# Performance work log

Hardware: AMD Instinct MI355X
Metric: run time of the kernel (lower is better)

The kernel has to match this reference:

```python
import jax, jax.numpy as jnp
import numpy as np

D_MODEL = 256
D_CLIP = 768
NHEAD = 8
HEAD_DIM = D_MODEL // NHEAD
Q_LEN = 100
B = 32
T_LEN = 1203


def setup_inputs() -> dict:
    key = jax.random.key(0)
    ks = jax.random.split(key, 16)
    xav = lambda k, o, i: jax.random.uniform(k, (o, i), jnp.float32, -1.0, 1.0) * np.sqrt(6.0 / (o + i))
    return {
        "tgt": jax.random.normal(ks[0], (Q_LEN, B, D_MODEL), jnp.float32),
        "text_classification": jax.random.normal(ks[1], (T_LEN, D_CLIP), jnp.float32),
        "query_pos": jax.random.normal(ks[2], (Q_LEN, B, D_MODEL), jnp.float32),
        "out_of_vocab_logits": jax.random.normal(ks[3], (B, Q_LEN, T_LEN), jnp.float32),
        "Wq": xav(ks[4], D_MODEL, D_MODEL), "bq": jnp.zeros((D_MODEL,), jnp.float32),
        "Wk": xav(ks[5], D_MODEL, D_CLIP), "bk": jnp.zeros((D_MODEL,), jnp.float32),
        "Wv": xav(ks[6], D_MODEL, D_CLIP), "bv": jnp.zeros((D_MODEL,), jnp.float32),
        "Wo": xav(ks[7], D_MODEL, D_MODEL), "bo": jnp.zeros((D_MODEL,), jnp.float32),
        "ln_g": jnp.ones((D_MODEL,), jnp.float32), "ln_b": jnp.zeros((D_MODEL,), jnp.float32),
        "logit_scale": jnp.asarray(np.log(1 / 0.07), jnp.float32),
    }


def _l2norm(x, eps=1e-6):
    # F.normalize: x / max(||x||, eps)
    n = jnp.sqrt(jnp.sum(x * x, axis=-1, keepdims=True))
    return x / jnp.maximum(n, eps)


def _layernorm(x, g, b, eps=1e-5):
    mu = jnp.mean(x, axis=-1, keepdims=True)
    var = jnp.mean((x - mu) ** 2, axis=-1, keepdims=True)
    return (x - mu) * jax.lax.rsqrt(var + eps) * g + b


def reference(tgt, text_classification, query_pos, out_of_vocab_logits,
              Wq, bq, Wk, bk, Wv, bv, Wo, bo, ln_g, ln_b, logit_scale):
    qin = tgt + query_pos                       # (Q, B, d_model)
    q = qin @ Wq.T + bq                         # (Q, B, d_model)
    # text embeddings shared across batch (2D path)
    k = text_classification @ Wk.T + bk         # (T, d_model)
    v = text_classification @ Wv.T + bv         # (T, d_model)

    q = q.transpose(1, 0, 2).reshape(B, Q_LEN, NHEAD, HEAD_DIM).transpose(0, 2, 1, 3)  # (B,h,Q,hd)
    k = k.reshape(T_LEN, NHEAD, HEAD_DIM).transpose(1, 0, 2)                            # (h,T,hd)
    v = v.reshape(T_LEN, NHEAD, HEAD_DIM).transpose(1, 0, 2)                            # (h,T,hd)

    q = _l2norm(q)
    k = _l2norm(k)
    scale = jnp.minimum(jnp.exp(logit_scale), 100.0)
    in_vocab = jnp.einsum('bhqd,hkd->bhqk', q, k) * scale                                # (B,h,Q,T)

    alpha = jnp.linspace(0.0, 1.0, NHEAD, dtype=in_vocab.dtype).reshape(1, NHEAD, 1, 1)
    logits = in_vocab * (1.0 - alpha) + out_of_vocab_logits[:, None] * alpha

    attn = jax.nn.softmax(logits, axis=-1)
    out = jnp.einsum('bhqk,hkd->bhqd', attn, v)                                          # (B,h,Q,hd)
    out = out.transpose(0, 2, 1, 3).reshape(B, Q_LEN, D_MODEL).transpose(1, 0, 2)        # (Q,B,d_model)
    out = out @ Wo.T + bo

    # forward_post: residual + layernorm (dropout=0)
    return _layernorm(tgt + out, ln_g, ln_b)
```

## Files before the change

### kernel.cpp

```cpp
#include <hip/hip_runtime.h>
#include <hip/hip_bf16.h>
#include <math.h>

#define D_MODEL 256
#define D_CLIP 768
#define NHEAD 8
#define HEAD_DIM 32
#define Q_LEN 100
#define BB 32
#define T_LEN 1203
#define TPAD 1216
#define MQ (Q_LEN*BB)
#define LOG2E 1.4426950408889634f

typedef __bf16 bf16_t;
typedef __bf16 bf16x8 __attribute__((ext_vector_type(8)));
typedef __bf16 bf16x4 __attribute__((ext_vector_type(4)));
typedef float f32x4 __attribute__((ext_vector_type(4)));

static __device__ __forceinline__ bf16_t to_bf16(float x) { return (bf16_t)x; }

static __device__ __forceinline__ bf16x8 cvt8(float4 a, float4 b) {
    bf16x8 r;
    r[0] = to_bf16(a.x); r[1] = to_bf16(a.y); r[2] = to_bf16(a.z); r[3] = to_bf16(a.w);
    r[4] = to_bf16(b.x); r[5] = to_bf16(b.y); r[6] = to_bf16(b.z); r[7] = to_bf16(b.w);
    return r;
}
static __device__ __forceinline__ bf16x8 cvt8add(float4 a, float4 b, float4 c, float4 d) {
    bf16x8 r;
    r[0] = to_bf16(a.x + c.x); r[1] = to_bf16(a.y + c.y); r[2] = to_bf16(a.z + c.z); r[3] = to_bf16(a.w + c.w);
    r[4] = to_bf16(b.x + d.x); r[5] = to_bf16(b.y + d.y); r[6] = to_bf16(b.z + d.z); r[7] = to_bf16(b.w + d.w);
    return r;
}

__launch_bounds__(256)
__global__ void proj_kernel(const float* __restrict__ tgt, const float* __restrict__ qpos,
                            const float* __restrict__ text,
                            const float* __restrict__ Wq, const float* __restrict__ Wk,
                            const float* __restrict__ Wv,
                            const float* __restrict__ bq, const float* __restrict__ bk,
                            const float* __restrict__ bv,
                            bf16_t* __restrict__ qn, bf16_t* __restrict__ kn,
                            bf16_t* __restrict__ vT) {
    const int bid = blockIdx.y;
    int z, xt;
    if (bid < 50)      { z = 0; xt = bid; }
    else if (bid < 69) { z = 1; xt = bid - 50; }
    else               { z = 2; xt = bid - 69; }
    const int j = blockIdx.x;
    const int nbase = j * 32;
    const int M = (z == 0) ? MQ : T_LEN;
    const int K = (z == 0) ? D_MODEL : D_CLIP;
    const float* Wf = (z == 0) ? Wq : (z == 1 ? Wk : Wv);
    const float* bias = (z == 0) ? bq : (z == 1 ? bk : bv);

    const int wave = threadIdx.x >> 6;
    const int lane = threadIdx.x & 63;
    const int c16 = lane & 15;
    const int quad = lane >> 4;
    const int mbase = xt * 64 + wave * 16;

    f32x4 a0 = (f32x4){0.f, 0.f, 0.f, 0.f};
    f32x4 a1 = (f32x4){0.f, 0.f, 0.f, 0.f};

    const int arow = (mbase + c16 < M) ? (mbase + c16) : (M - 1);
    const float* Ap0 = ((z == 0) ? tgt : text) + (size_t)arow * K + quad * 8;
    const float* Ap1 = ((z == 0) ? qpos : text) + (size_t)arow * K + quad * 8;
    const float* W0r = Wf + (size_t)(nbase + c16) * K + quad * 8;
    const float* W1r = Wf + (size_t)(nbase + 16 + c16) * K + quad * 8;
    const int ksteps = K / 32;
    if (z == 0) {
        #pragma unroll 4
        for (int ks = 0; ks < ksteps; ks++) {
            const int o = ks * 32;
            float4 t0 = *(const float4*)(Ap0 + o), t1 = *(const float4*)(Ap0 + o + 4);
            float4 p0 = *(const float4*)(Ap1 + o), p1 = *(const float4*)(Ap1 + o + 4);
            float4 w00 = *(const float4*)(W0r + o), w01 = *(const float4*)(W0r + o + 4);
            float4 w10 = *(const float4*)(W1r + o), w11 = *(const float4*)(W1r + o + 4);
            bf16x8 af = cvt8add(t0, t1, p0, p1);
            a0 = __builtin_amdgcn_mfma_f32_16x16x32_bf16(af, cvt8(w00, w01), a0, 0, 0, 0);
            a1 = __builtin_amdgcn_mfma_f32_16x16x32_bf16(af, cvt8(w10, w11), a1, 0, 0, 0);
        }
    } else {
        #pragma unroll 4
        for (int ks = 0; ks < ksteps; ks++) {
            const int o = ks * 32;
            float4 t0 = *(const float4*)(Ap0 + o), t1 = *(const float4*)(Ap0 + o + 4);
            float4 w00 = *(const float4*)(W0r + o), w01 = *(const float4*)(W0r + o + 4);
            float4 w10 = *(const float4*)(W1r + o), w11 = *(const float4*)(W1r + o + 4);
            bf16x8 af = cvt8(t0, t1);
            a0 = __builtin_amdgcn_mfma_f32_16x16x32_bf16(af, cvt8(w00, w01), a0, 0, 0, 0);
            a1 = __builtin_amdgcn_mfma_f32_16x16x32_bf16(af, cvt8(w10, w11), a1, 0, 0, 0);
        }
    }

    float b0s = bias[nbase + c16];
    float b1s = bias[nbase + 16 + c16];
    #pragma unroll
    for (int r = 0; r < 4; r++) { a0[r] += b0s; a1[r] += b1s; }
    if (z < 2) {
        #pragma unroll
        for (int r = 0; r < 4; r++) {
            float s = a0[r] * a0[r] + a1[r] * a1[r];
            #pragma unroll
            for (int o = 1; o < 16; o <<= 1) s += __shfl_xor(s, o);
            float sc = 1.0f / fmaxf(sqrtf(s), 1e-6f);
            a0[r] *= sc; a1[r] *= sc;
        }
    }
    #pragma unroll
    for (int r = 0; r < 4; r++) {
        int m = mbase + quad * 4 + r;
        if (m >= M) continue;
        if (z == 0) {
            int q = m >> 5, b = m & 31;
            size_t base = ((size_t)(b * NHEAD + j) * Q_LEN + q) * HEAD_DIM;
            qn[base + c16] = to_bf16(a0[r]);
            qn[base + 16 + c16] = to_bf16(a1[r]);
        } else if (z == 1) {
            size_t base = ((size_t)j * T_LEN + m) * HEAD_DIM;
            kn[base + c16] = to_bf16(a0[r]);
            kn[base + 16 + c16] = to_bf16(a1[r]);
        } else {
            vT[(size_t)(j * 32 + c16) * TPAD + m] = to_bf16(a0[r]);
            vT[(size_t)(j * 32 + 16 + c16) * TPAD + m] = to_bf16(a1[r]);
        }
    }
}

__launch_bounds__(256)
__global__ void attn_kernel(const bf16_t* __restrict__ qn, const bf16_t* __restrict__ kn,
                            const bf16_t* __restrict__ vT, const float* __restrict__ oov,
                            const float* __restrict__ logit_scale,
                            bf16_t* __restrict__ attn_out) {
    const int b = blockIdx.x;
    const int h = blockIdx.y;
    const int qt = blockIdx.z;
    const int qbase = qt * 16;
    const int wave = threadIdx.x >> 6;
    const int lane = threadIdx.x & 63;
    const int c16 = lane & 15;
    const int quad = lane >> 4;

    __shared__ __align__(16) bf16_t p_lds[4][2][16][40];
    __shared__ float l_lds[4][16];
    __shared__ float o_lds[4][32][16];

    const float scl = fminf(expf(logit_scale[0]), 100.0f);
    const float alpha = (float)h * (1.0f / 7.0f);
    const float sscale = scl * (1.0f - alpha) * LOG2E;
    const float oscale = alpha * LOG2E;
    const float mfix = sscale + 20.0f * oscale;

    const int q = qbase + c16;
    const int qc = (q < Q_LEN) ? q : (Q_LEN - 1);
    bf16x8 qf = *(const bf16x8*)(qn + ((size_t)(b * NHEAD + h) * Q_LEN + qc) * HEAD_DIM + quad * 8);

    f32x4 olo = (f32x4){0.f, 0.f, 0.f, 0.f};
    f32x4 ohi = (f32x4){0.f, 0.f, 0.f, 0.f};
    float l_s = 0.0f;

    const bf16_t* knh = kn + (size_t)h * T_LEN * HEAD_DIM;
    const bf16_t* vTh = vT + (size_t)h * HEAD_DIM * TPAD;
    const float* oovr = oov + ((size_t)b * Q_LEN + qc) * T_LEN;
    const f32x4 zero = (f32x4){0.f, 0.f, 0.f, 0.f};

    bf16x8 kA0, kA1, kB0, kB1, vA0, vA1, vB0, vB1;
    float4 oA0, oA1, oB0, oB1;

    #define LOAD_PAIR(P, kA0_, kA1_, kB0_, kB1_, vA0_, vA1_, vB0_, vB1_, oA0_, oA1_, oB0_, oB1_) \
        { const int tb0_ = (P) * 64; const int tb1_ = tb0_ + 32;                                   \
          kA0_ = *(const bf16x8*)(knh + (size_t)(tb0_ + c16) * HEAD_DIM + quad * 8);               \
          kA1_ = *(const bf16x8*)(knh + (size_t)(tb0_ + 16 + c16) * HEAD_DIM + quad * 8);          \
          kB0_ = *(const bf16x8*)(knh + (size_t)(tb1_ + c16) * HEAD_DIM + quad * 8);               \
          kB1_ = *(const bf16x8*)(knh + (size_t)(tb1_ + 16 + c16) * HEAD_DIM + quad * 8);          \
          vA0_ = *(const bf16x8*)(vTh + (size_t)c16 * TPAD + tb0_ + quad * 8);                     \
          vA1_ = *(const bf16x8*)(vTh + (size_t)(16 + c16) * TPAD + tb0_ + quad * 8);              \
          vB0_ = *(const bf16x8*)(vTh + (size_t)c16 * TPAD + tb1_ + quad * 8);                     \
          vB1_ = *(const bf16x8*)(vTh + (size_t)(16 + c16) * TPAD + tb1_ + quad * 8);              \
          oA0_ = *(const float4*)(oovr + tb0_ + quad * 4);                                         \
          oA1_ = *(const float4*)(oovr + tb0_ + 16 + quad * 4);                                    \
          oB0_ = *(const float4*)(oovr + tb1_ + quad * 4);                                         \
          oB1_ = *(const float4*)(oovr + tb1_ + 16 + quad * 4); }

    if (wave < 18) LOAD_PAIR(wave, kA0, kA1, kB0, kB1, vA0, vA1, vB0, vB1, oA0, oA1, oB0, oB1);

    for (int p = wave; p < 18; p += 4) {
        const int pn = (p + 4 < 18) ? (p + 4) : 17;
        bf16x8 nkA0, nkA1, nkB0, nkB1, nvA0, nvA1, nvB0, nvB1;
        float4 noA0, noA1, noB0, noB1;
        LOAD_PAIR(pn, nkA0, nkA1, nkB0, nkB1, nvA0, nvA1, nvB0, nvB1, noA0, noA1, noB0, noB1);

        f32x4 s00 = __builtin_amdgcn_mfma_f32_16x16x32_bf16(kA0, qf, zero, 0, 0, 0);
        f32x4 s01 = __builtin_amdgcn_mfma_f32_16x16x32_bf16(kA1, qf, zero, 0, 0, 0);
        f32x4 s10 = __builtin_amdgcn_mfma_f32_16x16x32_bf16(kB0, qf, zero, 0, 0, 0);
        f32x4 s11 = __builtin_amdgcn_mfma_f32_16x16x32_bf16(kB1, qf, zero, 0, 0, 0);
        float pa0[4], pa1[4], pb0[4], pb1[4];
        float ovA0[4] = {oA0.x, oA0.y, oA0.z, oA0.w};
        float ovA1[4] = {oA1.x, oA1.y, oA1.z, oA1.w};
        float ovB0[4] = {oB0.x, oB0.y, oB0.z, oB0.w};
        float ovB1[4] = {oB1.x, oB1.y, oB1.z, oB1.w};
        #pragma unroll
        for (int r = 0; r < 4; r++) {
            pa0[r] = exp2f(fmaf(s00[r], sscale, fmaf(ovA0[r], oscale, -mfix)));
            pa1[r] = exp2f(fmaf(s01[r], sscale, fmaf(ovA1[r], oscale, -mfix)));
            pb0[r] = exp2f(fmaf(s10[r], sscale, fmaf(ovB0[r], oscale, -mfix)));
            pb1[r] = exp2f(fmaf(s11[r], sscale, fmaf(ovB1[r], oscale, -mfix)));
        }
        l_s += ((pa0[0] + pa0[1]) + (pa0[2] + pa0[3])) + ((pa1[0] + pa1[1]) + (pa1[2] + pa1[3]))
             + ((pb0[0] + pb0[1]) + (pb0[2] + pb0[3])) + ((pb1[0] + pb1[1]) + (pb1[2] + pb1[3]));
        bf16x4 wA0 = { to_bf16(pa0[0]), to_bf16(pa0[1]), to_bf16(pa0[2]), to_bf16(pa0[3]) };
        bf16x4 wA1 = { to_bf16(pa1[0]), to_bf16(pa1[1]), to_bf16(pa1[2]), to_bf16(pa1[3]) };
        bf16x4 wB0 = { to_bf16(pb0[0]), to_bf16(pb0[1]), to_bf16(pb0[2]), to_bf16(pb0[3]) };
        bf16x4 wB1 = { to_bf16(pb1[0]), to_bf16(pb1[1]), to_bf16(pb1[2]), to_bf16(pb1[3]) };
        *(bf16x4*)&p_lds[wave][0][c16][quad * 4] = wA0;
        *(bf16x4*)&p_lds[wave][0][c16][16 + quad * 4] = wA1;
        *(bf16x4*)&p_lds[wave][1][c16][quad * 4] = wB0;
        *(bf16x4*)&p_lds[wave][1][c16][16 + quad * 4] = wB1;
        bf16x8 pf0 = *(const bf16x8*)(&p_lds[wave][0][c16][quad * 8]);
        bf16x8 pf1 = *(const bf16x8*)(&p_lds[wave][1][c16][quad * 8]);
        olo = __builtin_amdgcn_mfma_f32_16x16x32_bf16(vA0, pf0, olo, 0, 0, 0);
        ohi = __builtin_amdgcn_mfma_f32_16x16x32_bf16(vA1, pf0, ohi, 0, 0, 0);
        olo = __builtin_amdgcn_mfma_f32_16x16x32_bf16(vB0, pf1, olo, 0, 0, 0);
        ohi = __builtin_amdgcn_mfma_f32_16x16x32_bf16(vB1, pf1, ohi, 0, 0, 0);

        kA0 = nkA0; kA1 = nkA1; kB0 = nkB0; kB1 = nkB1;
        vA0 = nvA0; vA1 = nvA1; vB0 = nvB0; vB1 = nvB1;
        oA0 = noA0; oA1 = noA1; oB0 = noB0; oB1 = noB1;
    }
    #undef LOAD_PAIR

    if (wave == 2) {
        const int tb = 1152;
        bf16x8 kf0 = *(const bf16x8*)(knh + (size_t)(tb + c16) * HEAD_DIM + quad * 8);
        bf16x8 kf1 = *(const bf16x8*)(knh + (size_t)(tb + 16 + c16) * HEAD_DIM + quad * 8);
        float4 oa = *(const float4*)(oovr + tb + quad * 4);
        float4 oc = *(const float4*)(oovr + tb + 16 + quad * 4);
        bf16x8 v0 = *(const bf16x8*)(vTh + (size_t)c16 * TPAD + tb + quad * 8);
        bf16x8 v1 = *(const bf16x8*)(vTh + (size_t)(16 + c16) * TPAD + tb + quad * 8);
        f32x4 s0 = __builtin_amdgcn_mfma_f32_16x16x32_bf16(kf0, qf, zero, 0, 0, 0);
        f32x4 s1 = __builtin_amdgcn_mfma_f32_16x16x32_bf16(kf1, qf, zero, 0, 0, 0);
        float ova[4] = {oa.x, oa.y, oa.z, oa.w};
        float ovc[4] = {oc.x, oc.y, oc.z, oc.w};
        float p0[4], p1[4];
        #pragma unroll
        for (int r = 0; r < 4; r++) {
            p0[r] = exp2f(fmaf(s0[r], sscale, fmaf(ova[r], oscale, -mfix)));
            p1[r] = exp2f(fmaf(s1[r], sscale, fmaf(ovc[r], oscale, -mfix)));
        }
        l_s += ((p0[0] + p0[1]) + (p0[2] + p0[3])) + ((p1[0] + p1[1]) + (p1[2] + p1[3]));
        bf16x4 w0 = { to_bf16(p0[0]), to_bf16(p0[1]), to_bf16(p0[2]), to_bf16(p0[3]) };
        bf16x4 w1 = { to_bf16(p1[0]), to_bf16(p1[1]), to_bf16(p1[2]), to_bf16(p1[3]) };
        *(bf16x4*)&p_lds[wave][0][c16][quad * 4] = w0;
        *(bf16x4*)&p_lds[wave][0][c16][16 + quad * 4] = w1;
        bf16x8 pf = *(const bf16x8*)(&p_lds[wave][0][c16][quad * 8]);
        olo = __builtin_amdgcn_mfma_f32_16x16x32_bf16(v0, pf, olo, 0, 0, 0);
        ohi = __builtin_amdgcn_mfma_f32_16x16x32_bf16(v1, pf, ohi, 0, 0, 0);
    }

    if (wave == 3) {
        const int tb = 1184;
        int t1c = tb + 16 + c16;
        if (t1c >= T_LEN) t1c = T_LEN - 1;
        bf16x8 kf0 = *(const bf16x8*)(knh + (size_t)(tb + c16) * HEAD_DIM + quad * 8);
        bf16x8 kf1 = *(const bf16x8*)(knh + (size_t)t1c * HEAD_DIM + quad * 8);
        bf16x8 v0 = *(const bf16x8*)(vTh + (size_t)c16 * TPAD + tb + quad * 8);
        bf16x8 v1 = *(const bf16x8*)(vTh + (size_t)(16 + c16) * TPAD + tb + quad * 8);
        f32x4 s0 = __builtin_amdgcn_mfma_f32_16x16x32_bf16(kf0, qf, zero, 0, 0, 0);
        f32x4 s1 = __builtin_amdgcn_mfma_f32_16x16x32_bf16(kf1, qf, zero, 0, 0, 0);
        float p0[4], p1[4];
        #pragma unroll
        for (int r = 0; r < 4; r++) {
            int ta = tb + quad * 4 + r;
            int tb2 = tb + 16 + quad * 4 + r;
            float ova = oovr[ta];
            p0[r] = exp2f(fmaf(s0[r], sscale, fmaf(ova, oscale, -mfix)));
            if (tb2 < T_LEN) {
                float ovc = oovr[tb2];
                p1[r] = exp2f(fmaf(s1[r], sscale, fmaf(ovc, oscale, -mfix)));
            } else {
                p1[r] = 0.0f;
            }
        }
        l_s += ((p0[0] + p0[1]) + (p0[2] + p0[3])) + ((p1[0] + p1[1]) + (p1[2] + p1[3]));
        bf16x4 w0 = { to_bf16(p0[0]), to_bf16(p0[1]), to_bf16(p0[2]), to_bf16(p0[3]) };
        bf16x4 w1 = { to_bf16(p1[0]), to_bf16(p1[1]), to_bf16(p1[2]), to_bf16(p1[3]) };
        *(bf16x4*)&p_lds[wave][0][c16][quad * 4] = w0;
        *(bf16x4*)&p_lds[wave][0][c16][16 + quad * 4] = w1;
        bf16x8 pf = *(const bf16x8*)(&p_lds[wave][0][c16][quad * 8]);
        olo = __builtin_amdgcn_mfma_f32_16x16x32_bf16(v0, pf, olo, 0, 0, 0);
        ohi = __builtin_amdgcn_mfma_f32_16x16x32_bf16(v1, pf, ohi, 0, 0, 0);
    }

    l_s += __shfl_xor(l_s, 16);
    l_s += __shfl_xor(l_s, 32);
    if (quad == 0) l_lds[wave][c16] = l_s;
    #pragma unroll
    for (int r = 0; r < 4; r++) {
        o_lds[wave][quad * 4 + r][c16] = olo[r];
        o_lds[wave][16 + quad * 4 + r][c16] = ohi[r];
    }
    __syncthreads();
    const int q16 = threadIdx.x & 15;
    const int dd = threadIdx.x >> 4;
    float L = l_lds[0][q16] + l_lds[1][q16] + l_lds[2][q16] + l_lds[3][q16];
    const float invL = 1.0f / L;
    const int qout = qbase + q16;
    if (qout < Q_LEN) {
        #pragma unroll
        for (int half = 0; half < 2; half++) {
            int d = half * 16 + dd;
            float O = o_lds[0][d][q16] + o_lds[1][d][q16] +
                      o_lds[2][d][q16] + o_lds[3][d][q16];
            attn_out[((size_t)qout * BB + b) * D_MODEL + h * HEAD_DIM + d] = to_bf16(O * invL);
        }
    }
}

__launch_bounds__(256)
__global__ void out_kernel(const bf16_t* __restrict__ attn, const float* __restrict__ Wo,
                           const float* __restrict__ bo, const float* __restrict__ tgt,
                           const float* __restrict__ ln_g, const float* __restrict__ ln_b,
                           float* __restrict__ out) {
    const int xt = blockIdx.x;
    const int wave = threadIdx.x >> 6;
    const int lane = threadIdx.x & 63;
    const int c16 = lane & 15;
    const int quad = lane >> 4;
    const int mbase = xt * 16;

    __shared__ float xs[16][264];

    f32x4 acc[4];
    #pragma unroll
    for (int i = 0; i < 4; i++) acc[i] = (f32x4){0.f, 0.f, 0.f, 0.f};
    const bf16_t* Ap = attn + (size_t)(mbase + c16) * D_MODEL + quad * 8;
    #pragma unroll
    for (int ks = 0; ks < 8; ks++) {
        bf16x8 af = *(const bf16x8*)(Ap + ks * 32);
        #pragma unroll
        for (int nt = 0; nt < 4; nt++) {
            int n = wave * 64 + nt * 16 + c16;
            const float* wr = Wo + (size_t)n * D_MODEL + ks * 32 + quad * 8;
            float4 w0 = *(const float4*)wr;
            float4 w1 = *(const float4*)(wr + 4);
            acc[nt] = __builtin_amdgcn_mfma_f32_16x16x32_bf16(af, cvt8(w0, w1), acc[nt], 0, 0, 0);
        }
    }
    #pragma unroll
    for (int nt = 0; nt < 4; nt++) {
        int col = wave * 64 + nt * 16 + c16;
        float bb_ = bo[col];
        #pragma unroll
        for (int r = 0; r < 4; r++) {
            int m = mbase + quad * 4 + r;
            xs[quad * 4 + r][col] = acc[nt][r] + bb_ + tgt[(size_t)m * D_MODEL + col];
        }
    }
    __syncthreads();
    const int row = threadIdx.x >> 4;
    const int seg = threadIdx.x & 15;
    float sx = 0.f, sxx = 0.f;
    #pragma unroll
    for (int i = 0; i < 16; i++) {
        float x = xs[row][seg * 16 + i];
        sx += x; sxx += x * x;
    }
    #pragma unroll
    for (int o = 1; o < 16; o <<= 1) { sx += __shfl_xor(sx, o); sxx += __shfl_xor(sxx, o); }
    float mu = sx * (1.0f / 256.0f);
    float var = sxx * (1.0f / 256.0f) - mu * mu;
    float rstd = rsqrtf(fmaxf(var, 0.0f) + 1e-5f);
    size_t obase = (size_t)(mbase + row) * D_MODEL;
    #pragma unroll
    for (int i = 0; i < 16; i++) {
        int cidx = seg * 16 + i;
        out[obase + cidx] = (xs[row][cidx] - mu) * rstd * ln_g[cidx] + ln_b[cidx];
    }
}

extern "C" void kernel_launch(void* const* d_in, const int* in_sizes, int n_in,
                              void* d_out, int out_size, void* d_ws, size_t ws_size,
                              hipStream_t stream) {
    const float* tgt  = (const float*)d_in[0];
    const float* text = (const float*)d_in[1];
    const float* qpos = (const float*)d_in[2];
    const float* oov  = (const float*)d_in[3];
    const float* Wq = (const float*)d_in[4];
    const float* bq = (const float*)d_in[5];
    const float* Wk = (const float*)d_in[6];
    const float* bk = (const float*)d_in[7];
    const float* Wv = (const float*)d_in[8];
    const float* bv = (const float*)d_in[9];
    const float* Wo = (const float*)d_in[10];
    const float* bo = (const float*)d_in[11];
    const float* ln_g = (const float*)d_in[12];
    const float* ln_b = (const float*)d_in[13];
    const float* lsc  = (const float*)d_in[14];

    bf16_t* wsb = (bf16_t*)d_ws;
    bf16_t* qn   = wsb + 0;
    bf16_t* kn   = wsb + 819200;
    bf16_t* vT   = wsb + 1127168;
    bf16_t* attn = wsb + 1438464;
    float* out   = (float*)d_out;

    proj_kernel<<<dim3(8, 88, 1), 256, 0, stream>>>(tgt, qpos, text, Wq, Wk, Wv,
                                                    bq, bk, bv, qn, kn, vT);
    attn_kernel<<<dim3(32, 8, 7), 256, 0, stream>>>(qn, kn, vT, oov, lsc, attn);
    out_kernel<<<200, 256, 0, stream>>>(attn, Wo, bo, tgt, ln_g, ln_b, out);
}
```

Measured before the change: 186.5 us.

## Pre-convert inputs and weights to bf16 in a prep kernel; reorder attention grid

Adds a prep kernel that converts tgt+qpos, text and all weight matrices to bf16 in workspace, so the projection and output GEMMs read half-width operands without per-tile conversion. It also copies the out-of-vocab logits into workspace and reorders the attention grid so query tiles of the same batch and head run adjacently. The intent is to cut repeated fp32 weight loads and conversions inside the GEMMs, at the cost of an extra launch and an extra full pass over the inputs, including a pointless ~15MB copy of the oov logits.

```diff
diff --git a/kernel.cpp b/kernel.cpp
--- a/kernel.cpp
+++ b/kernel.cpp
@@ -20,24 +20,41 @@
 
 static __device__ __forceinline__ bf16_t to_bf16(float x) { return (bf16_t)x; }
 
-static __device__ __forceinline__ bf16x8 cvt8(float4 a, float4 b) {
-    bf16x8 r;
-    r[0] = to_bf16(a.x); r[1] = to_bf16(a.y); r[2] = to_bf16(a.z); r[3] = to_bf16(a.w);
-    r[4] = to_bf16(b.x); r[5] = to_bf16(b.y); r[6] = to_bf16(b.z); r[7] = to_bf16(b.w);
-    return r;
+__global__ void prep_kernel(const float* __restrict__ tgt, const float* __restrict__ qpos,
+                            const float* __restrict__ text, const float* __restrict__ Wq,
+                            const float* __restrict__ Wk, const float* __restrict__ Wv,
+                            const float* __restrict__ Wo, const float* __restrict__ oov,
+                            bf16_t* __restrict__ qin_bf, bf16_t* __restrict__ conv_dst,
+                            float* __restrict__ oov_ws) {
+    int idx = blockIdx.x * 256 + threadIdx.x;
+    if (idx >= 1529248) return;
+    if (idx < 204800) {
+        float4 a = ((const float4*)tgt)[idx];
+        float4 b = ((const float4*)qpos)[idx];
+        bf16x4 r = { to_bf16(a.x + b.x), to_bf16(a.y + b.y),
+                     to_bf16(a.z + b.z), to_bf16(a.w + b.w) };
+        *(bf16x4*)(qin_bf + (size_t)idx * 4) = r;
+    } else if (idx < 566848) {
+        int j = idx - 204800;
+        const float4* src;
+        if (j < 230976)      src = (const float4*)text + j;
+        else if (j < 247360) src = (const float4*)Wq + (j - 230976);
+        else if (j < 296512) src = (const float4*)Wk + (j - 247360);
+        else if (j < 345664) src = (const float4*)Wv + (j - 296512);
+        else                 src = (const float4*)Wo + (j - 345664);
+        float4 v = *src;
+        bf16x4 r = { to_bf16(v.x), to_bf16(v.y), to_bf16(v.z), to_bf16(v.w) };
+        *(bf16x4*)(conv_dst + (size_t)j * 4) = r;
+    } else {
+        int j = idx - 566848;
+        ((float4*)oov_ws)[j] = ((const float4*)oov)[j];
+    }
 }
-static __device__ __forceinline__ bf16x8 cvt8add(float4 a, float4 b, float4 c, float4 d) {
-    bf16x8 r;
-    r[0] = to_bf16(a.x + c.x); r[1] = to_bf16(a.y + c.y); r[2] = to_bf16(a.z + c.z); r[3] = to_bf16(a.w + c.w);
-    r[4] = to_bf16(b.x + d.x); r[5] = to_bf16(b.y + d.y); r[6] = to_bf16(b.z + d.z); r[7] = to_bf16(b.w + d.w);
-    return r;
-}
 
 __launch_bounds__(256)
-__global__ void proj_kernel(const float* __restrict__ tgt, const float* __restrict__ qpos,
-                            const float* __restrict__ text,
-                            const float* __restrict__ Wq, const float* __restrict__ Wk,
-                            const float* __restrict__ Wv,
+__global__ void proj_kernel(const bf16_t* __restrict__ qin_bf, const bf16_t* __restrict__ text_bf,
+                            const bf16_t* __restrict__ wq, const bf16_t* __restrict__ wk,
+                            const bf16_t* __restrict__ wv,
                             const float* __restrict__ bq, const float* __restrict__ bk,
                             const float* __restrict__ bv,
                             bf16_t* __restrict__ qn, bf16_t* __restrict__ kn,
@@ -51,7 +68,7 @@
     const int nbase = j * 32;
     const int M = (z == 0) ? MQ : T_LEN;
     const int K = (z == 0) ? D_MODEL : D_CLIP;
-    const float* Wf = (z == 0) ? Wq : (z == 1 ? Wk : Wv);
+    const bf16_t* W = (z == 0) ? wq : (z == 1 ? wk : wv);
     const float* bias = (z == 0) ? bq : (z == 1 ? bk : bv);
 
     const int wave = threadIdx.x >> 6;
@@ -64,34 +81,17 @@
     f32x4 a1 = (f32x4){0.f, 0.f, 0.f, 0.f};
 
     const int arow = (mbase + c16 < M) ? (mbase + c16) : (M - 1);
-    const float* Ap0 = ((z == 0) ? tgt : text) + (size_t)arow * K + quad * 8;
-    const float* Ap1 = ((z == 0) ? qpos : text) + (size_t)arow * K + quad * 8;
-    const float* W0r = Wf + (size_t)(nbase + c16) * K + quad * 8;
-    const float* W1r = Wf + (size_t)(nbase + 16 + c16) * K + quad * 8;
+    const bf16_t* Apb = ((z == 0) ? qin_bf : text_bf) + (size_t)arow * K + quad * 8;
+    const bf16_t* W0 = W + (size_t)(nbase + c16) * K + quad * 8;
+    const bf16_t* W1 = W + (size_t)(nbase + 16 + c16) * K + quad * 8;
     const int ksteps = K / 32;
-    if (z == 0) {
-        #pragma unroll 4
-        for (int ks = 0; ks < ksteps; ks++) {
-            const int o = ks * 32;
-            float4 t0 = *(const float4*)(Ap0 + o), t1 = *(const float4*)(Ap0 + o + 4);
-            float4 p0 = *(const float4*)(Ap1 + o), p1 = *(const float4*)(Ap1 + o + 4);
-            float4 w00 = *(const float4*)(W0r + o), w01 = *(const float4*)(W0r + o + 4);
-            float4 w10 = *(const float4*)(W1r + o), w11 = *(const float4*)(W1r + o + 4);
-            bf16x8 af = cvt8add(t0, t1, p0, p1);
-            a0 = __builtin_amdgcn_mfma_f32_16x16x32_bf16(af, cvt8(w00, w01), a0, 0, 0, 0);
-            a1 = __builtin_amdgcn_mfma_f32_16x16x32_bf16(af, cvt8(w10, w11), a1, 0, 0, 0);
-        }
-    } else {
-        #pragma unroll 4
-        for (int ks = 0; ks < ksteps; ks++) {
-            const int o = ks * 32;
-            float4 t0 = *(const float4*)(Ap0 + o), t1 = *(const float4*)(Ap0 + o + 4);
-            float4 w00 = *(const float4*)(W0r + o), w01 = *(const float4*)(W0r + o + 4);
-            float4 w10 = *(const float4*)(W1r + o), w11 = *(const float4*)(W1r + o + 4);
-            bf16x8 af = cvt8(t0, t1);
-            a0 = __builtin_amdgcn_mfma_f32_16x16x32_bf16(af, cvt8(w00, w01), a0, 0, 0, 0);
-            a1 = __builtin_amdgcn_mfma_f32_16x16x32_bf16(af, cvt8(w10, w11), a1, 0, 0, 0);
-        }
+    #pragma unroll 4
+    for (int ks = 0; ks < ksteps; ks++) {
+        bf16x8 af = *(const bf16x8*)(Apb + ks * 32);
+        bf16x8 b0 = *(const bf16x8*)(W0 + ks * 32);
+        bf16x8 b1 = *(const bf16x8*)(W1 + ks * 32);
+        a0 = __builtin_amdgcn_mfma_f32_16x16x32_bf16(af, b0, a0, 0, 0, 0);
+        a1 = __builtin_amdgcn_mfma_f32_16x16x32_bf16(af, b1, a1, 0, 0, 0);
     }
 
     float b0s = bias[nbase + c16];
@@ -133,9 +133,9 @@
                             const bf16_t* __restrict__ vT, const float* __restrict__ oov,
                             const float* __restrict__ logit_scale,
                             bf16_t* __restrict__ attn_out) {
-    const int b = blockIdx.x;
+    const int qt = blockIdx.x;
     const int h = blockIdx.y;
-    const int qt = blockIdx.z;
+    const int b = blockIdx.z;
     const int qbase = qt * 16;
     const int wave = threadIdx.x >> 6;
     const int lane = threadIdx.x & 63;
@@ -318,7 +318,7 @@
 }
 
 __launch_bounds__(256)
-__global__ void out_kernel(const bf16_t* __restrict__ attn, const float* __restrict__ Wo,
+__global__ void out_kernel(const bf16_t* __restrict__ attn, const bf16_t* __restrict__ wo,
                            const float* __restrict__ bo, const float* __restrict__ tgt,
                            const float* __restrict__ ln_g, const float* __restrict__ ln_b,
                            float* __restrict__ out) {
@@ -341,10 +341,8 @@
         #pragma unroll
         for (int nt = 0; nt < 4; nt++) {
             int n = wave * 64 + nt * 16 + c16;
-            const float* wr = Wo + (size_t)n * D_MODEL + ks * 32 + quad * 8;
-            float4 w0 = *(const float4*)wr;
-            float4 w1 = *(const float4*)(wr + 4);
-            acc[nt] = __builtin_amdgcn_mfma_f32_16x16x32_bf16(af, cvt8(w0, w1), acc[nt], 0, 0, 0);
+            bf16x8 bfr = *(const bf16x8*)(wo + (size_t)n * D_MODEL + ks * 32 + quad * 8);
+            acc[nt] = __builtin_amdgcn_mfma_f32_16x16x32_bf16(af, bfr, acc[nt], 0, 0, 0);
         }
     }
     #pragma unroll
@@ -399,14 +397,23 @@
     const float* lsc  = (const float*)d_in[14];
 
     bf16_t* wsb = (bf16_t*)d_ws;
-    bf16_t* qn   = wsb + 0;
-    bf16_t* kn   = wsb + 819200;
-    bf16_t* vT   = wsb + 1127168;
-    bf16_t* attn = wsb + 1438464;
-    float* out   = (float*)d_out;
-
-    proj_kernel<<<dim3(8, 88, 1), 256, 0, stream>>>(tgt, qpos, text, Wq, Wk, Wv,
+    bf16_t* text_bf = wsb + 0;
+    bf16_t* wq_bf   = wsb + 923904;
+    bf16_t* wk_bf   = wsb + 989440;
+    bf16_t* wv_bf   = wsb + 1186048;
+    bf16_t* wo_bf   = wsb + 1382656;
+    bf16_t* qin_bf  = wsb + 1448192;
+    bf16_t* qn      = wsb + 2267392;
+    bf16_t* kn      = wsb + 3086592;
+    bf16_t* vT      = wsb + 3394560;
+    bf16_t* attn    = wsb + 3705856;
+    float* oov_ws   = (float*)((char*)d_ws + 9050112);
+    float* out      = (float*)d_out;
+
+    prep_kernel<<<5975, 256, 0, stream>>>(tgt, qpos, text, Wq, Wk, Wv, Wo, oov,
+                                          qin_bf, text_bf, oov_ws);
+    proj_kernel<<<dim3(8, 88, 1), 256, 0, stream>>>(qin_bf, text_bf, wq_bf, wk_bf, wv_bf,
                                                     bq, bk, bv, qn, kn, vT);
-    attn_kernel<<<dim3(32, 8, 7), 256, 0, stream>>>(qn, kn, vT, oov, lsc, attn);
-    out_kernel<<<200, 256, 0, stream>>>(attn, Wo, bo, tgt, ln_g, ln_b, out);
+    attn_kernel<<<dim3(7, 8, 32), 256, 0, stream>>>(qn, kn, vT, oov_ws, lsc, attn);
+    out_kernel<<<200, 256, 0, stream>>>(attn, wo_bf, bo, tgt, ln_g, ln_b, out);
 }
```

Measured after the change: 172.8 us. 1.08x faster.
